# Optimization experiments

Measured on AMD Instinct MI355X. Metric: run time of the kernel, lower is better.

Reference implementation:

```python
import jax, jax.numpy as jnp
import numpy as np

N_NODES = 50000
N_EDGES = 400000
D = 64          # in/out channels (residual forces equality)
H = 8           # attention heads
L = 3           # number of GATv2 layers
NEG_SLOPE = 0.2
LN_EPS = 1e-5


def setup_inputs() -> dict:
    key = jax.random.key(0)
    ks = jax.random.split(key, 6)
    x = jax.random.normal(ks[0], (N_NODES, D), dtype=jnp.float32)
    edge_index = jax.random.randint(ks[1], (2, N_EDGES), 0, N_NODES, dtype=jnp.int64)
    scale = 1.0 / np.sqrt(D)
    Wl = jax.random.normal(ks[2], (L, D, H * D), dtype=jnp.float32) * scale
    Wr = jax.random.normal(ks[3], (L, D, H * D), dtype=jnp.float32) * scale
    att = jax.random.normal(ks[4], (L, H, D), dtype=jnp.float32) * 0.1
    b = jnp.zeros((L, D), dtype=jnp.float32)
    gamma = jnp.ones((L, D), dtype=jnp.float32)
    beta = jnp.zeros((L, D), dtype=jnp.float32)
    return {"x": x, "Wl": Wl, "Wr": Wr, "att": att, "b": b,
            "gamma": gamma, "beta": beta, "edge_index": edge_index}


def _gatv2_stack(x, Wl, Wr, att, b, gamma, beta, src, dst, num_nodes):
    # src/dst already include self-loops (PyG add_self_loops=True)
    for l in range(Wl.shape[0]):
        xl = (x @ Wl[l]).reshape(num_nodes, H, -1)   # [N,H,C] messages (source transform)
        xr = (x @ Wr[l]).reshape(num_nodes, H, -1)   # [N,H,C] target transform
        m = jax.nn.leaky_relu(xl[src] + xr[dst], NEG_SLOPE)       # [E,H,C]
        e = jnp.einsum('ehc,hc->eh', m, att[l])                    # [E,H]
        # segment softmax over incoming edges of each target node
        emax = jax.ops.segment_max(e, dst, num_segments=num_nodes)
        ex = jnp.exp(e - emax[dst])
        denom = jax.ops.segment_sum(ex, dst, num_segments=num_nodes)
        alpha = ex / denom[dst]                                    # [E,H]
        agg = jax.ops.segment_sum(alpha[:, :, None] * xl[src], dst,
                                  num_segments=num_nodes)          # [N,H,C]
        h = agg.mean(axis=1) + b[l]                                # concat=False -> head mean, + bias
        x = h + x                                                  # residual
        mu = x.mean(-1, keepdims=True)
        var = x.var(-1, keepdims=True)
        x = (x - mu) / jnp.sqrt(var + LN_EPS) * gamma[l] + beta[l] # LayerNorm
        x = jax.nn.relu(x)
    return x


def reference(x, Wl, Wr, att, b, gamma, beta, edge_index):
    num_nodes = x.shape[0]
    loops = jnp.arange(num_nodes, dtype=edge_index.dtype)
    src = jnp.concatenate([edge_index[0], loops])
    dst = jnp.concatenate([edge_index[1], loops])
    return _gatv2_stack(x, Wl, Wr, att, b, gamma, beta, src, dst, num_nodes)
```

## Files before the change

kernel.cpp:

```cpp
#include <hip/hip_runtime.h>

#define N_NODES 50000
#define N_EDGES 400000
#define EP (N_EDGES + N_NODES)
#define D 64
#define H 8
#define NEG_SLOPE 0.2f
#define LN_EPS 1e-5f
#define CHUNK 196
#define SCAN_BLOCKS 256
#define PAD_N 50048
#define GEMM_BLOCKS (782 * 8)
#define LOG2E 1.4426950408889634f

typedef unsigned short ushort_t;
typedef unsigned int uint_t;
typedef __attribute__((ext_vector_type(8))) short short8;
typedef __attribute__((ext_vector_type(4))) float f32x4;
typedef __attribute__((ext_vector_type(2))) float f32x2;

#if defined(__has_builtin)
#if __has_builtin(__builtin_amdgcn_cvt_pk_bf16_f32)
#define HAVE_CVT_PK_BF16 1
#endif
#endif

__device__ __forceinline__ ushort_t f2bf(float f) {
    uint_t u = __float_as_uint(f);
    u += 0x7fffu + ((u >> 16) & 1u);
    return (ushort_t)(u >> 16);
}
__device__ __forceinline__ uint_t pack_bf2(float a, float b) {
#ifdef HAVE_CVT_PK_BF16
    typedef __attribute__((ext_vector_type(2))) __bf16 bf16x2_t;
    bf16x2_t v = __builtin_amdgcn_cvt_pk_bf16_f32(a, b);
    uint_t r;
    __builtin_memcpy(&r, &v, 4);
    return r;
#else
    return (uint_t)f2bf(a) | ((uint_t)f2bf(b) << 16);
#endif
}
__device__ __forceinline__ f32x2 mkf2(uint_t u) {
    f32x2 r;
    r.x = __uint_as_float(u << 16);
    r.y = __uint_as_float(u & 0xffff0000u);
    return r;
}

__device__ __forceinline__ f32x2 pk_add(f32x2 a, f32x2 b) {
    f32x2 d;
    asm("v_pk_add_f32 %0, %1, %2" : "=v"(d) : "v"(a), "v"(b));
    return d;
}
__device__ __forceinline__ f32x2 pk_mul(f32x2 a, f32x2 b) {
    f32x2 d;
    asm("v_pk_mul_f32 %0, %1, %2" : "=v"(d) : "v"(a), "v"(b));
    return d;
}
__device__ __forceinline__ f32x2 pk_fma(f32x2 a, f32x2 b, f32x2 c) {
    f32x2 d;
    asm("v_pk_fma_f32 %0, %1, %2, %3" : "=v"(d) : "v"(a), "v"(b), "v"(c));
    return d;
}
__device__ __forceinline__ f32x2 pk_abs(f32x2 a) {
    f32x2 r;
    r.x = __uint_as_float(__float_as_uint(a.x) & 0x7fffffffu);
    r.y = __uint_as_float(__float_as_uint(a.y) & 0x7fffffffu);
    return r;
}

__device__ __forceinline__ float xor1_dpp(float x) {
    int i = __float_as_int(x);
    return __int_as_float(__builtin_amdgcn_update_dpp(i, i, 0xB1, 0xF, 0xF, 1));
}
__device__ __forceinline__ float xor2_dpp(float x) {
    int i = __float_as_int(x);
    return __int_as_float(__builtin_amdgcn_update_dpp(i, i, 0x4E, 0xF, 0xF, 1));
}
__device__ __forceinline__ float xor8_dpp(float x) {
    int i = __float_as_int(x);
    return __int_as_float(__builtin_amdgcn_update_dpp(i, i, 0x128, 0xF, 0xF, 1));
}
__device__ __forceinline__ float xor4_swz(float x) {
    return __int_as_float(__builtin_amdgcn_ds_swizzle(__float_as_int(x), 0x101F));
}
__device__ __forceinline__ float xor16_swz(float x) {
    return __int_as_float(__builtin_amdgcn_ds_swizzle(__float_as_int(x), 0x401F));
}

__device__ __forceinline__ void edge_sd(const int* __restrict__ ei, int eid, int& s, int& d) {
    if (eid < N_EDGES) { s = ei[eid]; d = ei[N_EDGES + eid]; }
    else               { s = d = eid - N_EDGES; }
}


__global__ __launch_bounds__(256) void setup_all(const int* __restrict__ ei, int* __restrict__ counts,
                                                 const float* __restrict__ x,
                                                 const float* __restrict__ Wl, const float* __restrict__ Wr,
                                                 ushort_t* __restrict__ xb, ushort_t* __restrict__ Wt) {
    int t = blockIdx.x * 256 + threadIdx.x;
    if (t < EP) {
        int s, d; edge_sd(ei, t, s, d);
        atomicAdd(&counts[d], 1);
        return;
    }
    t -= EP;
    if (t < N_NODES * 64) { xb[t] = f2bf(x[t]); return; }
    t -= N_NODES * 64;
    if (t >= 3 * 1024 * 64) return;
    int l = t >> 16, rem = t & 65535, col = rem >> 6, k = rem & 63;
    float v = (col < 512) ? Wl[((size_t)l * 64 + k) * 512 + col]
                          : Wr[((size_t)l * 64 + k) * 512 + (col - 512)];
    Wt[t] = f2bf(v);
}


__global__ __launch_bounds__(256) void csr_scan1(const int* __restrict__ counts, int* __restrict__ bsum,
                                                 int* __restrict__ bhist) {
    __shared__ int sd[256];
    __shared__ int hist[64];
    int t = threadIdx.x, b = blockIdx.x;
    if (t < 64) hist[t] = 0;
    int idx = b * CHUNK + t;
    int v = (t < CHUNK && idx < N_NODES) ? counts[idx] : 0;
    sd[t] = v;
    __syncthreads();
    if (t < CHUNK && idx < N_NODES) atomicAdd(&hist[63 - min(v, 63)], 1);
    for (int d = 128; d > 0; d >>= 1) {
        __syncthreads();
        if (t < d) sd[t] += sd[t + d];
    }
    __syncthreads();
    if (t == 0) bsum[b] = sd[0];
    if (t < 64) bhist[b * 64 + t] = hist[t];
}

__global__ __launch_bounds__(256) void csr_scan2(int* __restrict__ bsum,
                                                 const int* __restrict__ bhist, int* __restrict__ pbase) {
    __shared__ int sd[256];
    __shared__ int sg[64 * 4];
    __shared__ int base[64];
    int t = threadIdx.x;
    sd[t] = bsum[t];
    __syncthreads();
    for (int d = 1; d < 256; d <<= 1) {
        int v = (t >= d) ? sd[t - d] : 0;
        __syncthreads();
        if (t >= d) sd[t] += v;
        __syncthreads();
    }
    bsum[t] = (t > 0) ? sd[t - 1] : 0;

    int k = t & 63, g = t >> 6;
    int s = 0;
    for (int j = 0; j < 64; ++j) s += bhist[(g * 64 + j) * 64 + k];
    sg[k * 4 + g] = s;
    __syncthreads();
    if (t == 0) {
        int run = 0;
        for (int kk = 0; kk < 64; ++kk) {
            base[kk] = run;
            run += sg[kk * 4 + 0] + sg[kk * 4 + 1] + sg[kk * 4 + 2] + sg[kk * 4 + 3];
        }
    }
    __syncthreads();
    int run = base[k];
    for (int gg = 0; gg < g; ++gg) run += sg[k * 4 + gg];
    for (int j = 0; j < 64; ++j) {
        int b = g * 64 + j;
        pbase[b * 64 + k] = run;
        run += bhist[b * 64 + k];
    }
}

__global__ __launch_bounds__(256) void csr_scan3(const int* __restrict__ counts, const int* __restrict__ bsum,
                                                 int* __restrict__ offsets, int* __restrict__ cursor,
                                                 const int* __restrict__ pbase, int* __restrict__ node_order) {
    __shared__ int sd[256];
    __shared__ int cur[64];
    int t = threadIdx.x, b = blockIdx.x;
    if (t < 64) cur[t] = pbase[b * 64 + t];
    int idx = b * CHUNK + t;
    int v = (t < CHUNK && idx < N_NODES) ? counts[idx] : 0;
    sd[t] = v;
    __syncthreads();
    for (int d = 1; d < 256; d <<= 1) {
        int u = (t >= d) ? sd[t - d] : 0;
        __syncthreads();
        if (t >= d) sd[t] += u;
        __syncthreads();
    }
    if (t < CHUNK && idx < N_NODES) {
        int ex = bsum[b] + sd[t] - v;
        offsets[idx] = ex;
        cursor[idx]  = ex;
        int bin = 63 - min(v, 63);
        int p = atomicAdd(&cur[bin], 1);
        node_order[p] = idx;
    }
    if (b == 0 && t == 0) offsets[N_NODES] = EP;
}

__global__ __launch_bounds__(256) void gemm_mfma(const ushort_t* __restrict__ xb,
                                                 const ushort_t* __restrict__ Wt,
                                                 ushort_t* __restrict__ xlr,
                                                 const int* __restrict__ ei, int* __restrict__ cursor,
                                                 int* __restrict__ csr_src) {
    __shared__ ushort_t sW[128 * 72];
    int b = blockIdx.x;
    if (b >= GEMM_BLOCKS) {
        int t = (b - GEMM_BLOCKS) * 256 + threadIdx.x;
        if (t >= EP) return;
        int s, d; edge_sd(ei, t, s, d);
        int pos = atomicAdd(&cursor[d], 1);
        csr_src[pos] = s;
        return;
    }
    int colq = b / 782;
    int bx = b - colq * 782;
    int t = threadIdx.x;
    const ushort_t* Wg = Wt + (size_t)colq * 128 * 64;
    {
        int col = t >> 1, half = t & 1;
        const uint4* g = (const uint4*)(Wg + col * 64 + half * 32);
        uint4* l = (uint4*)(sW + col * 72 + half * 32);
        l[0] = g[0]; l[1] = g[1]; l[2] = g[2]; l[3] = g[3];
    }
    __syncthreads();
    int lane = t & 63, w = t >> 6;
    int ln = lane & 15, q = lane >> 4;
    int node = bx * 64 + w * 16 + ln;
    int nclamp = node < N_NODES ? node : N_NODES - 1;
    const short8 b0 = *(const short8*)(xb + (size_t)nclamp * 64 + q * 8);
    const short8 b1 = *(const short8*)(xb + (size_t)nclamp * 64 + 32 + q * 8);
#pragma unroll
    for (int ct = 0; ct < 8; ++ct) {
        const short8 a0 = *(const short8*)(sW + (ct * 16 + ln) * 72 + q * 8);
        const short8 a1 = *(const short8*)(sW + (ct * 16 + ln) * 72 + 32 + q * 8);
        f32x4 acc = {0.f, 0.f, 0.f, 0.f};
        acc = __builtin_amdgcn_mfma_f32_16x16x32_bf16(a0, b0, acc, 0, 0, 0);
        acc = __builtin_amdgcn_mfma_f32_16x16x32_bf16(a1, b1, acc, 0, 0, 0);
        if (node < N_NODES) {
            uint_t lo = pack_bf2(acc[0], acc[1]);
            uint_t hi = pack_bf2(acc[2], acc[3]);
            *(uint2*)(xlr + (size_t)node * 1024 + colq * 128 + ct * 16 + q * 4) = make_uint2(lo, hi);
        }
    }
}

__global__ __launch_bounds__(256) void node_fused(const float* __restrict__ x_in,
                                                  const ushort_t* __restrict__ xlr,
                                                  const float* __restrict__ att,
                                                  const int* __restrict__ offsets, const int* __restrict__ csr_src,
                                                  const int* __restrict__ node_order,
                                                  const float* __restrict__ bias, const float* __restrict__ gamma,
                                                  const float* __restrict__ beta, float* __restrict__ x_out,
                                                  ushort_t* __restrict__ xb_out) {
    int n = node_order[blockIdx.x * 4 + (threadIdx.x >> 6)];
    n = __builtin_amdgcn_readfirstlane(n);
    int lane = threadIdx.x & 63;
    int h = lane >> 3, i = lane & 7;
    int beg = __builtin_amdgcn_readfirstlane(offsets[n]);
    int end = __builtin_amdgcn_readfirstlane(offsets[n + 1]);
    int off = h * 64 + i * 8;

    uint4 ru = *(const uint4*)(xlr + (size_t)n * 1024 + 512 + off);
    f32x2 rv0 = mkf2(ru.x), rv1 = mkf2(ru.y), rv2 = mkf2(ru.z), rv3 = mkf2(ru.w);
    const float4* pa = (const float4*)(att + h * 64 + i * 8);
    float4 aa = pa[0], ab = pa[1];
    f32x2 a0 = {aa.x, aa.y}, a1 = {aa.z, aa.w}, a2 = {ab.x, ab.y}, a3 = {ab.z, ab.w};
    f32x2 a60 = (0.6f * LOG2E) * a0, a61 = (0.6f * LOG2E) * a1,
          a62 = (0.6f * LOG2E) * a2, a63 = (0.6f * LOG2E) * a3;
    f32x2 a40 = (0.4f * LOG2E) * a0, a41 = (0.4f * LOG2E) * a1,
          a42 = (0.4f * LOG2E) * a2, a43 = (0.4f * LOG2E) * a3;

    float den = 0.f;
    f32x2 acc0 = {0.f, 0.f}, acc1 = {0.f, 0.f}, acc2 = {0.f, 0.f}, acc3 = {0.f, 0.f};

#define PROCESS(cur)                                                     \
    {                                                                    \
        f32x2 v0 = mkf2(cur.x), v1 = mkf2(cur.y),                        \
              v2 = mkf2(cur.z), v3 = mkf2(cur.w);                        \
        f32x2 p = pk_mul(a60, v0);                                       \
        p = pk_fma(a61, v1, p);                                          \
        p = pk_fma(a62, v2, p);                                          \
        p = pk_fma(a63, v3, p);                                          \
        p = pk_fma(a40, pk_abs(pk_add(v0, rv0)), p);                     \
        p = pk_fma(a41, pk_abs(pk_add(v1, rv1)), p);                     \
        p = pk_fma(a42, pk_abs(pk_add(v2, rv2)), p);                     \
        p = pk_fma(a43, pk_abs(pk_add(v3, rv3)), p);                     \
        float pdot = p.x + p.y;                                          \
        pdot += xor1_dpp(pdot);                                          \
        pdot += xor2_dpp(pdot);                                          \
        pdot += xor4_swz(pdot);                                          \
        float wgt = __builtin_exp2f(pdot);                               \
        den += wgt;                                                      \
        f32x2 wv = {wgt, wgt};                                           \
        acc0 = pk_fma(wv, v0, acc0);                                     \
        acc1 = pk_fma(wv, v1, acc1);                                     \
        acc2 = pk_fma(wv, v2, acc2);                                     \
        acc3 = pk_fma(wv, v3, acc3);                                     \
    }

    for (int base = beg; base < end; base += 64) {
        int idx = base + lane;
        int srcs = csr_src[idx < end ? idx : end - 1];
        int cnt = min(64, end - base);
        int j = 0;
        for (; j + 8 <= cnt; j += 8) {
            uint4 q[8];
#pragma unroll
            for (int u = 0; u < 8; ++u) {
                int ss = __shfl(srcs, j + u);
                q[u] = *(const uint4*)(xlr + (size_t)ss * 1024 + off);
            }
#pragma unroll
            for (int u = 0; u < 8; ++u) PROCESS(q[u]);
        }
        for (; j < cnt; ++j) {
            int ss = __shfl(srcs, j);
            uint4 qq = *(const uint4*)(xlr + (size_t)ss * 1024 + off);
            PROCESS(qq);
        }
    }
#undef PROCESS

    float invden = 0.125f / den;
    f32x2 iv = {invden, invden};
    acc0 = pk_mul(acc0, iv); acc1 = pk_mul(acc1, iv);
    acc2 = pk_mul(acc2, iv); acc3 = pk_mul(acc3, iv);
    float acc[8] = {acc0.x, acc0.y, acc1.x, acc1.y, acc2.x, acc2.y, acc3.x, acc3.y};
#pragma unroll
    for (int k2 = 0; k2 < 8; ++k2) {
        acc[k2] += xor8_dpp(acc[k2]);
        acc[k2] += xor16_swz(acc[k2]);
        acc[k2] += __shfl_xor(acc[k2], 32);
    }

    int cbase = i * 8;
    const float4* px = (const float4*)(x_in + n * 64 + cbase);
    float4 x0 = px[0], x1 = px[1];
    float xi[8] = {x0.x, x0.y, x0.z, x0.w, x1.x, x1.y, x1.z, x1.w};
    float v[8];
    float sum = 0.f, sq = 0.f;
#pragma unroll
    for (int k2 = 0; k2 < 8; ++k2) {
        float val = acc[k2] + bias[cbase + k2] + xi[k2];
        v[k2] = val; sum += val; sq += val * val;
    }
    sum += xor1_dpp(sum); sq += xor1_dpp(sq);
    sum += xor2_dpp(sum); sq += xor2_dpp(sq);
    sum += xor4_swz(sum); sq += xor4_swz(sq);
    float mu   = sum * (1.0f / 64.0f);
    float var  = sq * (1.0f / 64.0f) - mu * mu;
    float rstd = rsqrtf(var + LN_EPS);

    if (h == 0) {
        float o[8];
#pragma unroll
        for (int k2 = 0; k2 < 8; ++k2) {
            float y = (v[k2] - mu) * rstd * gamma[cbase + k2] + beta[cbase + k2];
            o[k2] = fmaxf(y, 0.f);
        }
        float4* po = (float4*)(x_out + n * 64 + cbase);
        po[0] = make_float4(o[0], o[1], o[2], o[3]);
        po[1] = make_float4(o[4], o[5], o[6], o[7]);
        *(uint4*)(xb_out + (size_t)n * 64 + cbase) =
            make_uint4(pack_bf2(o[0], o[1]), pack_bf2(o[2], o[3]),
                       pack_bf2(o[4], o[5]), pack_bf2(o[6], o[7]));
    }
}


extern "C" void kernel_launch(void* const* d_in, const int* in_sizes, int n_in,
                              void* d_out, int out_size, void* d_ws, size_t ws_size,
                              hipStream_t stream) {
    const float* x     = (const float*)d_in[0];
    const float* Wl    = (const float*)d_in[1];
    const float* Wr    = (const float*)d_in[2];
    const float* att   = (const float*)d_in[3];
    const float* b     = (const float*)d_in[4];
    const float* gamma = (const float*)d_in[5];
    const float* beta  = (const float*)d_in[6];
    const int*   ei    = (const int*)d_in[7];
    float* out = (float*)d_out;

    ushort_t* xlr = (ushort_t*)d_ws;
    ushort_t* xb  = xlr + (size_t)N_NODES * 1024;
    ushort_t* Wt  = xb + (size_t)PAD_N * 64;
    int* counts     = (int*)(Wt + 3 * 1024 * 64);
    int* offsets    = counts + PAD_N;
    int* cursor     = offsets + PAD_N;
    int* bsum       = cursor + PAD_N;
    int* node_order = bsum + 256;
    int* bhist      = node_order + PAD_N;
    int* pbase      = bhist + SCAN_BLOCKS * 64;
    int* csr_src    = pbase + SCAN_BLOCKS * 64;

    hipMemsetAsync(counts, 0, N_NODES * sizeof(int), stream);

    int setup_threads = EP + N_NODES * 64 + 3 * 1024 * 64;
    setup_all<<<(setup_threads + 255) / 256, 256, 0, stream>>>(ei, counts, x, Wl, Wr, xb, Wt);

    csr_scan1<<<SCAN_BLOCKS, 256, 0, stream>>>(counts, bsum, bhist);
    csr_scan2<<<1, 256, 0, stream>>>(bsum, bhist, pbase);
    csr_scan3<<<SCAN_BLOCKS, 256, 0, stream>>>(counts, bsum, offsets, cursor, pbase, node_order);

    int eb = (EP + 255) / 256;
    const float* xin = x;
    for (int l = 0; l < 3; ++l) {
        int grid = (l == 0) ? GEMM_BLOCKS + eb : GEMM_BLOCKS;
        gemm_mfma <<<grid, 256, 0, stream>>>(xb, Wt + (size_t)l * 1024 * 64, xlr, ei, cursor, csr_src);
        node_fused<<<N_NODES / 4, 256, 0, stream>>>(xin, xlr, att + l * (H * D), offsets, csr_src,
                                                    node_order, b + l * D, gamma + l * D, beta + l * D,
                                                    out, xb);
        xin = out;
    }
}
```

Before: 465.7 us.

## Store source-transformed features in FP8 and pack per-node CSR descriptors

The GEMM now writes the xl half of the projection as FP8 (e4m3 via cvt_pk_fp8) into its own buffer and keeps xr in bf16 in a separate buffer. The edge-gather loop in node_fused reads 8 bytes per lane instead of 16, aiming to halve the random-gather traffic that dominates the aggregation. Node order and CSR offsets are merged into one int4 descriptor per node, which removes the dependent offsets lookups, and launch bounds now request higher occupancy. FP8 quantization of the messages lowers precision of both the attention logits and the aggregation, which could threaten the tolerance check.

```diff
diff --git a/kernel.cpp b/kernel.cpp
--- a/kernel.cpp
+++ b/kernel.cpp
@@ -15,6 +15,7 @@
 
 typedef unsigned short ushort_t;
 typedef unsigned int uint_t;
+typedef unsigned char uchar_t;
 typedef __attribute__((ext_vector_type(8))) short short8;
 typedef __attribute__((ext_vector_type(4))) float f32x4;
 typedef __attribute__((ext_vector_type(2))) float f32x2;
@@ -47,6 +48,12 @@
     r.y = __uint_as_float(u & 0xffff0000u);
     return r;
 }
+template <bool HI>
+__device__ __forceinline__ f32x2 cvt8(uint_t u) {
+    typedef __attribute__((ext_vector_type(2))) float v2f;
+    v2f r = __builtin_amdgcn_cvt_pk_f32_fp8((int)u, HI);
+    return (f32x2){r.x, r.y};
+}
 
 __device__ __forceinline__ f32x2 pk_add(f32x2 a, f32x2 b) {
     f32x2 d;
@@ -175,8 +182,8 @@
 }
 
 __global__ __launch_bounds__(256) void csr_scan3(const int* __restrict__ counts, const int* __restrict__ bsum,
-                                                 int* __restrict__ offsets, int* __restrict__ cursor,
-                                                 const int* __restrict__ pbase, int* __restrict__ node_order) {
+                                                 int* __restrict__ cursor,
+                                                 const int* __restrict__ pbase, int4* __restrict__ desc) {
     __shared__ int sd[256];
     __shared__ int cur[64];
     int t = threadIdx.x, b = blockIdx.x;
@@ -193,18 +200,16 @@
     }
     if (t < CHUNK && idx < N_NODES) {
         int ex = bsum[b] + sd[t] - v;
-        offsets[idx] = ex;
-        cursor[idx]  = ex;
+        cursor[idx] = ex;
         int bin = 63 - min(v, 63);
         int p = atomicAdd(&cur[bin], 1);
-        node_order[p] = idx;
-    }
-    if (b == 0 && t == 0) offsets[N_NODES] = EP;
+        desc[p] = make_int4(idx, ex, ex + v, 0);
+    }
 }
 
 __global__ __launch_bounds__(256) void gemm_mfma(const ushort_t* __restrict__ xb,
                                                  const ushort_t* __restrict__ Wt,
-                                                 ushort_t* __restrict__ xlr,
+                                                 uchar_t* __restrict__ xl8, ushort_t* __restrict__ xr16,
                                                  const int* __restrict__ ei, int* __restrict__ cursor,
                                                  int* __restrict__ csr_src) {
     __shared__ ushort_t sW[128 * 72];
@@ -242,30 +247,38 @@
         acc = __builtin_amdgcn_mfma_f32_16x16x32_bf16(a0, b0, acc, 0, 0, 0);
         acc = __builtin_amdgcn_mfma_f32_16x16x32_bf16(a1, b1, acc, 0, 0, 0);
         if (node < N_NODES) {
-            uint_t lo = pack_bf2(acc[0], acc[1]);
-            uint_t hi = pack_bf2(acc[2], acc[3]);
-            *(uint2*)(xlr + (size_t)node * 1024 + colq * 128 + ct * 16 + q * 4) = make_uint2(lo, hi);
+            int cbase = ct * 16 + q * 4;
+            if (colq < 4) {
+                int r = 0;
+                r = __builtin_amdgcn_cvt_pk_fp8_f32(acc[0], acc[1], r, false);
+                r = __builtin_amdgcn_cvt_pk_fp8_f32(acc[2], acc[3], r, true);
+                *(uint_t*)(xl8 + (size_t)node * 512 + colq * 128 + cbase) = (uint_t)r;
+            } else {
+                uint_t lo = pack_bf2(acc[0], acc[1]);
+                uint_t hi = pack_bf2(acc[2], acc[3]);
+                *(uint2*)(xr16 + (size_t)node * 512 + (colq - 4) * 128 + cbase) = make_uint2(lo, hi);
+            }
         }
     }
 }
 
-__global__ __launch_bounds__(256) void node_fused(const float* __restrict__ x_in,
-                                                  const ushort_t* __restrict__ xlr,
+__global__ __launch_bounds__(256, 8) void node_fused(const float* __restrict__ x_in,
+                                                  const uchar_t* __restrict__ xl8,
+                                                  const ushort_t* __restrict__ xr16,
                                                   const float* __restrict__ att,
-                                                  const int* __restrict__ offsets, const int* __restrict__ csr_src,
-                                                  const int* __restrict__ node_order,
+                                                  const int4* __restrict__ desc, const int* __restrict__ csr_src,
                                                   const float* __restrict__ bias, const float* __restrict__ gamma,
                                                   const float* __restrict__ beta, float* __restrict__ x_out,
                                                   ushort_t* __restrict__ xb_out) {
-    int n = node_order[blockIdx.x * 4 + (threadIdx.x >> 6)];
-    n = __builtin_amdgcn_readfirstlane(n);
+    int4 dd = desc[blockIdx.x * 4 + (threadIdx.x >> 6)];
+    int n   = __builtin_amdgcn_readfirstlane(dd.x);
+    int beg = __builtin_amdgcn_readfirstlane(dd.y);
+    int end = __builtin_amdgcn_readfirstlane(dd.z);
     int lane = threadIdx.x & 63;
     int h = lane >> 3, i = lane & 7;
-    int beg = __builtin_amdgcn_readfirstlane(offsets[n]);
-    int end = __builtin_amdgcn_readfirstlane(offsets[n + 1]);
-    int off = h * 64 + i * 8;
-
-    uint4 ru = *(const uint4*)(xlr + (size_t)n * 1024 + 512 + off);
+    int off8 = h * 64 + i * 8;
+
+    uint4 ru = *(const uint4*)(xr16 + (size_t)n * 512 + off8);
     f32x2 rv0 = mkf2(ru.x), rv1 = mkf2(ru.y), rv2 = mkf2(ru.z), rv3 = mkf2(ru.w);
     const float4* pa = (const float4*)(att + h * 64 + i * 8);
     float4 aa = pa[0], ab = pa[1];
@@ -280,8 +293,8 @@
 
 #define PROCESS(cur)                                                     \
     {                                                                    \
-        f32x2 v0 = mkf2(cur.x), v1 = mkf2(cur.y),                        \
-              v2 = mkf2(cur.z), v3 = mkf2(cur.w);                        \
+        f32x2 v0 = cvt8<false>(cur.x), v1 = cvt8<true>(cur.x),           \
+              v2 = cvt8<false>(cur.y), v3 = cvt8<true>(cur.y);           \
         f32x2 p = pk_mul(a60, v0);                                       \
         p = pk_fma(a61, v1, p);                                          \
         p = pk_fma(a62, v2, p);                                          \
@@ -309,18 +322,18 @@
         int cnt = min(64, end - base);
         int j = 0;
         for (; j + 8 <= cnt; j += 8) {
-            uint4 q[8];
+            uint2 q[8];
 #pragma unroll
             for (int u = 0; u < 8; ++u) {
                 int ss = __shfl(srcs, j + u);
-                q[u] = *(const uint4*)(xlr + (size_t)ss * 1024 + off);
+                q[u] = *(const uint2*)(xl8 + (size_t)ss * 512 + off8);
             }
 #pragma unroll
             for (int u = 0; u < 8; ++u) PROCESS(q[u]);
         }
         for (; j < cnt; ++j) {
             int ss = __shfl(srcs, j);
-            uint4 qq = *(const uint4*)(xlr + (size_t)ss * 1024 + off);
+            uint2 qq = *(const uint2*)(xl8 + (size_t)ss * 512 + off8);
             PROCESS(qq);
         }
     }
@@ -386,17 +399,17 @@
     const int*   ei    = (const int*)d_in[7];
     float* out = (float*)d_out;
 
-    ushort_t* xlr = (ushort_t*)d_ws;
-    ushort_t* xb  = xlr + (size_t)N_NODES * 1024;
-    ushort_t* Wt  = xb + (size_t)PAD_N * 64;
-    int* counts     = (int*)(Wt + 3 * 1024 * 64);
-    int* offsets    = counts + PAD_N;
-    int* cursor     = offsets + PAD_N;
-    int* bsum       = cursor + PAD_N;
-    int* node_order = bsum + 256;
-    int* bhist      = node_order + PAD_N;
-    int* pbase      = bhist + SCAN_BLOCKS * 64;
-    int* csr_src    = pbase + SCAN_BLOCKS * 64;
+    uchar_t* xl8   = (uchar_t*)d_ws;
+    ushort_t* xr16 = (ushort_t*)(xl8 + (size_t)PAD_N * 512);
+    ushort_t* xb   = xr16 + (size_t)PAD_N * 512;
+    ushort_t* Wt   = xb + (size_t)PAD_N * 64;
+    int* counts    = (int*)(Wt + 3 * 1024 * 64);
+    int* cursor    = counts + PAD_N;
+    int* bsum      = cursor + PAD_N;
+    int* bhist     = bsum + 256;
+    int* pbase     = bhist + SCAN_BLOCKS * 64;
+    int4* desc     = (int4*)(pbase + SCAN_BLOCKS * 64);
+    int* csr_src   = (int*)(desc + PAD_N);
 
     hipMemsetAsync(counts, 0, N_NODES * sizeof(int), stream);
 
@@ -405,15 +418,15 @@
 
     csr_scan1<<<SCAN_BLOCKS, 256, 0, stream>>>(counts, bsum, bhist);
     csr_scan2<<<1, 256, 0, stream>>>(bsum, bhist, pbase);
-    csr_scan3<<<SCAN_BLOCKS, 256, 0, stream>>>(counts, bsum, offsets, cursor, pbase, node_order);
+    csr_scan3<<<SCAN_BLOCKS, 256, 0, stream>>>(counts, bsum, cursor, pbase, desc);
 
     int eb = (EP + 255) / 256;
     const float* xin = x;
     for (int l = 0; l < 3; ++l) {
         int grid = (l == 0) ? GEMM_BLOCKS + eb : GEMM_BLOCKS;
-        gemm_mfma <<<grid, 256, 0, stream>>>(xb, Wt + (size_t)l * 1024 * 64, xlr, ei, cursor, csr_src);
-        node_fused<<<N_NODES / 4, 256, 0, stream>>>(xin, xlr, att + l * (H * D), offsets, csr_src,
-                                                    node_order, b + l * D, gamma + l * D, beta + l * D,
+        gemm_mfma <<<grid, 256, 0, stream>>>(xb, Wt + (size_t)l * 1024 * 64, xl8, xr16, ei, cursor, csr_src);
+        node_fused<<<N_NODES / 4, 256, 0, stream>>>(xin, xl8, xr16, att + l * (H * D), desc, csr_src,
+                                                    b + l * D, gamma + l * D, beta + l * D,
                                                     out, xb);
         xin = out;
     }
```

Result: faster. 430.9 us (-7.5%).
